# Kernel optimization log

Measured on AMD Instinct MI355X. Metric: run time of the kernel, lower is better.

The kernel has to match this reference:

```python
import jax, jax.numpy as jnp
import numpy as np

NORMALIZED_LENGTH = 1.0
LOSS_WEIGHTS = (0.25, 1.0)
EPS = 1e-12  # matches torch F.normalize eps


def setup_inputs() -> dict:
    key = jax.random.key(0)
    k1, k2 = jax.random.split(key)
    x = jax.random.normal(k1, (16, 128, 64, 64), dtype=jnp.float32)
    codebook = jax.random.normal(k2, (1024, 128), dtype=jnp.float32)
    return {"x": x, "codebook": codebook}


def _forward(x, codebook):
    # --- VQCodebook.forward: normalize x along channel dim (dim=1) ---
    # NOTE: the torch source's codebook renormalization uses non-in-place
    # .div/.mul whose results are discarded, so the codebook is unchanged.
    if NORMALIZED_LENGTH > 0:
        nrm = jnp.linalg.norm(x, axis=1, keepdims=True)  # [B,1,H,W]
        x = NORMALIZED_LENGTH * x / jnp.maximum(nrm, EPS)

    B, C, H, W = x.shape
    z = jnp.transpose(x, (0, 2, 3, 1)).reshape(-1, C)  # [N, C], N = B*H*W

    # Pairwise squared L2 distances via ||z||^2 - 2 z c^T + ||c||^2.
    # argmin of squared distance == argmin of distance.
    z2 = jnp.sum(z * z, axis=1, keepdims=True)             # [N, 1]
    c2 = jnp.sum(codebook * codebook, axis=1)              # [K]
    d2 = z2 - 2.0 * jnp.einsum('nc,kc->nk', z, codebook) + c2[None, :]  # [N, K]
    idx = jnp.argmin(d2, axis=1)                           # [N]

    q = codebook[idx]                                      # [N, C]
    q = q.reshape(B, H, W, C).transpose(0, 3, 1, 2)        # [B, C, H, W]

    lw0, lw1 = LOSS_WEIGHTS
    diff_codebook = jax.lax.stop_gradient(x) - q
    diff_commit = x - jax.lax.stop_gradient(q)
    loss0 = lw0 * jnp.mean(jnp.linalg.norm(diff_codebook, axis=1))
    loss1 = lw1 * jnp.mean(jnp.linalg.norm(diff_commit, axis=1))
    return q, loss0, loss1


def reference(x, codebook):
    return _forward(x, codebook)
```

## Files before the change

### kernel.cpp

```cpp
#include <hip/hip_runtime.h>
#include <math.h>

#define K_CODES 1024
#define C_DIM   128
#define HW      4096
#define CHW     (C_DIM*HW)
#define N_POS   65536
#define Q_ELEMS 8388608

#define WS_S    0
#define WS_C2   256
#define WS_IDX  8192


typedef __attribute__((ext_vector_type(8))) short short8;
typedef __attribute__((ext_vector_type(4))) float f32x4;

__device__ __forceinline__ unsigned short f2bf(float f) {
    unsigned u = __float_as_uint(f);
    u += 0x7FFFu + ((u >> 16) & 1u);
    return (unsigned short)(u >> 16);
}

__device__ __forceinline__ void gll16(const void* g, void* l) {
    __builtin_amdgcn_global_load_lds(
        (const __attribute__((address_space(1))) void*)g,
        (__attribute__((address_space(3))) void*)l, 16, 0, 0);
}

__global__ void prep_kernel(const float* __restrict__ cb, float* __restrict__ ws,
                            unsigned short* __restrict__ cbbf) {
    __shared__ __align__(16) unsigned short srow[128];
    int k = blockIdx.x;
    int l = threadIdx.x;
    if (k == 0 && l == 0) *(float*)((char*)ws + WS_S) = 0.f;
    float v1 = cb[k * C_DIM + l];
    float v2 = cb[k * C_DIM + 64 + l];
    int c1 = l, c2 = 64 + l;
    srow[(((c1 >> 3) ^ (k & 7)) << 3) | (c1 & 7)] = f2bf(v1);
    srow[(((c2 >> 3) ^ (k & 7)) << 3) | (c2 & 7)] = f2bf(v2);
    float ss = v1 * v1 + v2 * v2;
    #pragma unroll
    for (int off = 32; off > 0; off >>= 1) ss += __shfl_down(ss, off);
    if (l == 0) ((float*)((char*)ws + WS_C2))[k] = ss;
    __syncthreads();
    if (l < 16) ((uint4*)cbbf)[k * 16 + l] = ((const uint4*)srow)[l];
}

__global__ __launch_bounds__(256, 2) void vq_mfma(const float* __restrict__ x,
                                                  const float* __restrict__ cb,
                                                  const unsigned short* __restrict__ cbbf,
                                                  const float* __restrict__ c2w,
                                                  int* __restrict__ idxw,
                                                  float* __restrict__ Sw) {
    __shared__ __align__(16) unsigned short cbuf[2 * 1024 * 8];
    __shared__ float mbuf[2][2][16][3];

    const int t  = threadIdx.x;
    const int w  = t >> 6;
    const int kh = w & 1;
    const int pg = w >> 1;
    const int ln = t & 63;
    const int lp = ln & 15;
    const int q  = ln >> 4;
    const int bid = blockIdx.x;
    const int b   = bid >> 6;
    const int s0  = (bid & 63) << 6;

    short8 xf[2][4];
    float  r2v[2];
    {
        float ss[2] = {0.f, 0.f};
        #pragma unroll
        for (int pt = 0; pt < 2; ++pt) {
            const float* xgp = x + b * CHW + s0 + pg * 32 + pt * 16 + lp;
            #pragma unroll
            for (int cs = 0; cs < 4; ++cs) {
                union { short8 v; unsigned short u[8]; } fu;
                #pragma unroll
                for (int j = 0; j < 8; ++j) {
                    float vv = xgp[(32 * cs + 8 * q + j) * HW];
                    ss[pt] = fmaf(vv, vv, ss[pt]);
                    fu.u[j] = f2bf(vv);
                }
                xf[pt][cs] = fu.v;
            }
        }
        #pragma unroll
        for (int pt = 0; pt < 2; ++pt) {
            float s = ss[pt];
            s += __shfl_xor(s, 16);
            s += __shfl_xor(s, 32);
            r2v[pt] = -2.0f / fmaxf(sqrtf(s), 1e-12f);
        }
    }

    const float FMAX = __uint_as_float(0x7F7FFFFFu);
    float m1[2] = {FMAX, FMAX}, m2[2] = {FMAX, FMAX}, m3[2] = {FMAX, FMAX};

    const char* gbase = (const char*)cbbf + (kh * 512) * 256 + (pg * 512 + ln) * 16;
    char* lbase = (char*)cbuf + (kh * 1024 + pg * 512) * 16;

    #pragma unroll
    for (int r = 0; r < 8; ++r)
        gll16(gbase + r * 1024, lbase + r * 1024);
    __syncthreads();

    for (int i = 0; i < 8; ++i) {
        const int k0 = kh * 512 + i * 64;

        f32x4 acc[4][2];
        #pragma unroll
        for (int ct = 0; ct < 4; ++ct)
            #pragma unroll
            for (int pt = 0; pt < 2; ++pt) acc[ct][pt] = 0;

        const unsigned short* cbp = cbuf + kh * 8192;
        #pragma unroll
        for (int cs = 0; cs < 4; ++cs) {
            short8 ah[4];
            #pragma unroll
            for (int ct = 0; ct < 4; ++ct) {
                int g = (16 * ct + lp) * 16 + ((4 * cs + q) ^ (lp & 7));
                ah[ct] = *(const short8*)(cbp + g * 8);
            }
            #pragma unroll
            for (int ct = 0; ct < 4; ++ct)
                #pragma unroll
                for (int pt = 0; pt < 2; ++pt)
                    acc[ct][pt] = __builtin_amdgcn_mfma_f32_16x16x32_bf16(
                        ah[ct], xf[pt][cs], acc[ct][pt], 0, 0, 0);
        }

        #pragma unroll
        for (int ct = 0; ct < 4; ++ct) {
            float4 c2vv = *(const float4*)(c2w + k0 + 16 * ct + 4 * q);
            float c2a[4] = {c2vv.x, c2vv.y, c2vv.z, c2vv.w};
            const int kb0 = k0 + 16 * ct + 4 * q;
            #pragma unroll
            for (int pt = 0; pt < 2; ++pt) {
                #pragma unroll
                for (int reg = 0; reg < 4; ++reg) {
                    float s = fmaf(r2v[pt], acc[ct][pt][reg], c2a[reg]);
                    unsigned pb = (__float_as_uint(s) & 0xFFFFFC00u) |
                                  (unsigned)(kb0 + reg);
                    float u  = __uint_as_float(pb);
                    float t3 = __builtin_amdgcn_fmed3f(m2[pt], m3[pt], u);
                    float t2 = __builtin_amdgcn_fmed3f(m1[pt], m2[pt], u);
                    m1[pt] = fminf(m1[pt], u); m2[pt] = t2; m3[pt] = t3;
                }
            }
        }

        if (i < 7) {
            __syncthreads();
            #pragma unroll
            for (int r = 0; r < 8; ++r)
                gll16(gbase + (i + 1) * 16384 + r * 1024, lbase + r * 1024);
            __syncthreads();
        }
    }

    #pragma unroll
    for (int d = 16; d <= 32; d <<= 1) {
        #pragma unroll
        for (int pt = 0; pt < 2; ++pt) {
            float o1 = __shfl_xor(m1[pt], d), o2 = __shfl_xor(m2[pt], d),
                  o3 = __shfl_xor(m3[pt], d);
            float u, t2, t3;
            u = o1; t3 = __builtin_amdgcn_fmed3f(m2[pt], m3[pt], u);
            t2 = __builtin_amdgcn_fmed3f(m1[pt], m2[pt], u);
            m1[pt] = fminf(m1[pt], u); m2[pt] = t2; m3[pt] = t3;
            u = o2; t3 = __builtin_amdgcn_fmed3f(m2[pt], m3[pt], u);
            t2 = __builtin_amdgcn_fmed3f(m1[pt], m2[pt], u);
            m1[pt] = fminf(m1[pt], u); m2[pt] = t2; m3[pt] = t3;
            u = o3; t3 = __builtin_amdgcn_fmed3f(m2[pt], m3[pt], u);
            t2 = __builtin_amdgcn_fmed3f(m1[pt], m2[pt], u);
            m1[pt] = fminf(m1[pt], u); m2[pt] = t2; m3[pt] = t3;
        }
    }

    if (kh == 1 && ln < 16) {
        #pragma unroll
        for (int pt = 0; pt < 2; ++pt) {
            mbuf[pg][pt][lp][0] = m1[pt];
            mbuf[pg][pt][lp][1] = m2[pt];
            mbuf[pg][pt][lp][2] = m3[pt];
        }
    }
    __syncthreads();

    if (kh == 0) {
        float lsum = 0.f;
        #pragma unroll
        for (int pt = 0; pt < 2; ++pt) {
            #pragma unroll
            for (int c = 0; c < 3; ++c) {
                float u  = mbuf[pg][pt][lp][c];
                float t3 = __builtin_amdgcn_fmed3f(m2[pt], m3[pt], u);
                float t2 = __builtin_amdgcn_fmed3f(m1[pt], m2[pt], u);
                m1[pt] = fminf(m1[pt], u); m2[pt] = t2; m3[pt] = t3;
            }
            int ks[3] = {(int)(__float_as_uint(m1[pt]) & 1023u),
                         (int)(__float_as_uint(m2[pt]) & 1023u),
                         (int)(__float_as_uint(m3[pt]) & 1023u)};

            float xr[32];
            const float* xgp = x + b * CHW + s0 + pg * 32 + pt * 16 + lp;
            #pragma unroll
            for (int cs = 0; cs < 4; ++cs)
                #pragma unroll
                for (int j = 0; j < 8; ++j)
                    xr[cs * 8 + j] = xgp[(32 * cs + 8 * q + j) * HW];

            float dots[3];
            #pragma unroll
            for (int jj = 0; jj < 3; ++jj) {
                const float* crow = cb + ks[jj] * C_DIM + 8 * q;
                float p = 0.f;
                #pragma unroll
                for (int cs = 0; cs < 4; ++cs) {
                    float4 a0 = *(const float4*)(crow + 32 * cs);
                    float4 a1 = *(const float4*)(crow + 32 * cs + 4);
                    p = fmaf(xr[cs*8+0], a0.x, p); p = fmaf(xr[cs*8+1], a0.y, p);
                    p = fmaf(xr[cs*8+2], a0.z, p); p = fmaf(xr[cs*8+3], a0.w, p);
                    p = fmaf(xr[cs*8+4], a1.x, p); p = fmaf(xr[cs*8+5], a1.y, p);
                    p = fmaf(xr[cs*8+6], a1.z, p); p = fmaf(xr[cs*8+7], a1.w, p);
                }
                p += __shfl_xor(p, 16);
                p += __shfl_xor(p, 32);
                dots[jj] = p;
            }
            float sb = fmaf(r2v[pt], dots[0], c2w[ks[0]]); int kb = ks[0];
            float s2 = fmaf(r2v[pt], dots[1], c2w[ks[1]]);
            if (s2 < sb || (s2 == sb && ks[1] < kb)) { sb = s2; kb = ks[1]; }
            float s3 = fmaf(r2v[pt], dots[2], c2w[ks[2]]);
            if (s3 < sb || (s3 == sb && ks[2] < kb)) { sb = s3; kb = ks[2]; }

            if (ln < 16) idxw[bid * 64 + pg * 32 + pt * 16 + lp] = kb;
            lsum += sqrtf(fmaxf(1.0f + sb, 0.f));
        }
        #pragma unroll
        for (int off = 32; off > 0; off >>= 1) lsum += __shfl_down(lsum, off);
        if (ln == 0) atomicAdd(Sw, 0.25f * lsum);
    }
}

__global__ void write_q(const float* __restrict__ cb,
                        const int* __restrict__ idxw,
                        const float* __restrict__ ws,
                        float* __restrict__ out) {
    int id = blockIdx.x * 256 + threadIdx.x;
    int p  = id & (N_POS - 1);
    int c4 = id >> 16;
    int b  = p >> 12, s = p & 4095;
    int row = idxw[p];
    float4 v = ((const float4*)cb)[row * 32 + c4];
    float* o = out + b * CHW + (c4 * 4) * HW + s;
    o[0]      = v.x;
    o[HW]     = v.y;
    o[2 * HW] = v.z;
    o[3 * HW] = v.w;
    if (id == 0) {
        float S = *(const float*)((const char*)ws + WS_S);
        float m = S / (float)N_POS;
        out[Q_ELEMS]     = 0.25f * m;
        out[Q_ELEMS + 1] = m;
    }
}

extern "C" void kernel_launch(void* const* d_in, const int* in_sizes, int n_in,
                              void* d_out, int out_size, void* d_ws, size_t ws_size,
                              hipStream_t stream) {
    const float* x  = (const float*)d_in[0];
    const float* cb = (const float*)d_in[1];
    float* out = (float*)d_out;
    float* ws  = (float*)d_ws;

    const float* c2w = (const float*)((const char*)d_ws + WS_C2);
    int*  idxw = (int*)((char*)d_ws + WS_IDX);
    float* Sw  = (float*)((char*)d_ws + WS_S);
    unsigned short* cbbf = (unsigned short*)d_out;

    prep_kernel<<<K_CODES, 64, 0, stream>>>(cb, ws, cbbf);
    vq_mfma    <<<N_POS / 64, 256, 0, stream>>>(x, cb, cbbf, c2w, idxw, Sw);
    write_q    <<<Q_ELEMS / 1024, 256, 0, stream>>>(cb, idxw, ws, out);
}
```

Before: 72.85 us.

## Fuse quantized-output gather into VQ kernel, leave batch 0 to separate pass

The main MFMA kernel now stores each block's argmin indices in shared memory and writes the gathered codebook rows straight into the output for every batch except batch 0. Batch 0 is excluded because its output region holds the bf16 codebook copy that other blocks are still reading. A smaller follow-up kernel writes only batch 0 plus the loss scalars. This removes most of the separate gather kernel's index reads and launch work, but the output stores now run inside the compute kernel and add a block barrier there.

```diff
diff --git a/kernel.cpp b/kernel.cpp
--- a/kernel.cpp
+++ b/kernel.cpp
@@ -52,9 +52,11 @@
                                                   const unsigned short* __restrict__ cbbf,
                                                   const float* __restrict__ c2w,
                                                   int* __restrict__ idxw,
-                                                  float* __restrict__ Sw) {
+                                                  float* __restrict__ Sw,
+                                                  float* __restrict__ out) {
     __shared__ __align__(16) unsigned short cbuf[2 * 1024 * 8];
     __shared__ float mbuf[2][2][16][3];
+    __shared__ int ibuf[64];
 
     const int t  = threadIdx.x;
     const int w  = t >> 6;
@@ -237,26 +239,44 @@
             float s3 = fmaf(r2v[pt], dots[2], c2w[ks[2]]);
             if (s3 < sb || (s3 == sb && ks[2] < kb)) { sb = s3; kb = ks[2]; }
 
-            if (ln < 16) idxw[bid * 64 + pg * 32 + pt * 16 + lp] = kb;
+            if (ln < 16) {
+                idxw[bid * 64 + pg * 32 + pt * 16 + lp] = kb;
+                ibuf[pg * 32 + pt * 16 + lp] = kb;
+            }
             lsum += sqrtf(fmaxf(1.0f + sb, 0.f));
         }
         #pragma unroll
         for (int off = 32; off > 0; off >>= 1) lsum += __shfl_down(lsum, off);
         if (ln == 0) atomicAdd(Sw, 0.25f * lsum);
     }
-}
-
-__global__ void write_q(const float* __restrict__ cb,
-                        const int* __restrict__ idxw,
-                        const float* __restrict__ ws,
-                        float* __restrict__ out) {
+
+    __syncthreads();
+    if (b != 0) {
+        const int row = ibuf[ln];
+        const float4* cbr = (const float4*)cb + row * 32;
+        float* ob = out + b * CHW + s0 + ln;
+        #pragma unroll
+        for (int c4 = w * 8; c4 < w * 8 + 8; ++c4) {
+            float4 v = cbr[c4];
+            float* o = ob + (c4 * 4) * HW;
+            o[0]      = v.x;
+            o[HW]     = v.y;
+            o[2 * HW] = v.z;
+            o[3 * HW] = v.w;
+        }
+    }
+}
+
+__global__ void write_q0(const float* __restrict__ cb,
+                         const int* __restrict__ idxw,
+                         const float* __restrict__ ws,
+                         float* __restrict__ out) {
     int id = blockIdx.x * 256 + threadIdx.x;
-    int p  = id & (N_POS - 1);
-    int c4 = id >> 16;
-    int b  = p >> 12, s = p & 4095;
-    int row = idxw[p];
+    int s  = id & 4095;
+    int c4 = id >> 12;
+    int row = idxw[s];
     float4 v = ((const float4*)cb)[row * 32 + c4];
-    float* o = out + b * CHW + (c4 * 4) * HW + s;
+    float* o = out + (c4 * 4) * HW + s;
     o[0]      = v.x;
     o[HW]     = v.y;
     o[2 * HW] = v.z;
@@ -283,6 +303,6 @@
     unsigned short* cbbf = (unsigned short*)d_out;
 
     prep_kernel<<<K_CODES, 64, 0, stream>>>(cb, ws, cbbf);
-    vq_mfma    <<<N_POS / 64, 256, 0, stream>>>(x, cb, cbbf, c2w, idxw, Sw);
-    write_q    <<<Q_ELEMS / 1024, 256, 0, stream>>>(cb, idxw, ws, out);
-}
+    vq_mfma    <<<N_POS / 64, 256, 0, stream>>>(x, cb, cbbf, c2w, idxw, Sw, out);
+    write_q0   <<<512, 256, 0, stream>>>(cb, idxw, ws, out);
+}
```

Result: faster. 70.66 us (-3.0%).
